# Kernel optimization log

Hardware: AMD Instinct MI355X
Metric: run time of the kernel (lower is better)

Reference implementation:

```python
import jax, jax.numpy as jnp
import numpy as np

N_NODES = 100000
N_EDGES = 1600000
D_FEAT = 32


def setup_inputs() -> dict:
    key = jax.random.key(0)
    k1, k2, k3 = jax.random.split(key, 3)
    features = jax.random.normal(k1, (N_NODES, D_FEAT), dtype=jnp.float32)
    src = jax.random.randint(k2, (N_EDGES,), 0, N_NODES, dtype=jnp.int64)
    dst = jax.random.randint(k3, (N_EDGES,), 0, N_NODES, dtype=jnp.int64)
    return {"features": features, "src": src, "dst": dst}


def reference(features, src, dst):
    # LightConv with norm='both' (default): symmetric degree normalization.
    n = features.shape[0]
    # out-degrees (number of edges leaving each node)
    deg = jnp.zeros((n,), dtype=features.dtype).at[src].add(1.0)
    # norm = deg^-0.5 with inf -> 0 for isolated nodes
    norm = jnp.where(deg > 0, jax.lax.rsqrt(jnp.maximum(deg, 1.0)), 0.0)[:, None]  # [N,1]
    # pre-scale (norm in ['left','both'])
    x = features * norm
    # message = copy_src, reduce = sum over incoming edges
    agg = jax.ops.segment_sum(x[src], dst, num_segments=n)  # [N,D]
    # post-scale (norm in ['right','both']) -- original reads srcdata['norm'],
    # which is the same per-node norm array for a homogeneous graph.
    return agg * norm
```

## Files before the change

kernel.cpp:

```cpp
#include <hip/hip_runtime.h>

#define D_FEAT 32
#define NPB 256
#define NPB_SHIFT 8
#define KMAX 512
#define BPART 512
#define TPART 256
#define SRC_BITS 17
#define SRC_MASK 0x1FFFF
#define CAPI 6144


__global__ __launch_bounds__(TPART) void partition_atomic(const int* __restrict__ src,
                                                          const int* __restrict__ dst,
                                                          int* __restrict__ cntD_g,
                                                          int* __restrict__ cntS_g,
                                                          int* __restrict__ routed_d,
                                                          unsigned char* __restrict__ routed_b,
                                                          int n_edges, int K) {
    __shared__ int hD[KMAX];
    __shared__ int hS[KMAX];
    __shared__ int bD[KMAX];
    __shared__ int bS[KMAX];
    int b = blockIdx.x;
    int tid = threadIdx.x;
    for (int i = tid; i < K; i += TPART) { hD[i] = 0; hS[i] = 0; }
    __syncthreads();
    int chunk = (((n_edges + BPART - 1) / BPART) + 3) & ~3;
    int base = b * chunk;
    int eend = min(base + chunk, n_edges);
    int nvec = (eend > base) ? ((eend - base) >> 2) : 0;
    const int4* d4p = (const int4*)(dst + base);
    const int4* s4p = (const int4*)(src + base);
    for (int i = tid; i < nvec; i += TPART) {
        int4 d4 = d4p[i];
        int4 s4 = s4p[i];
        atomicAdd(&hD[d4.x >> NPB_SHIFT], 1);
        atomicAdd(&hD[d4.y >> NPB_SHIFT], 1);
        atomicAdd(&hD[d4.z >> NPB_SHIFT], 1);
        atomicAdd(&hD[d4.w >> NPB_SHIFT], 1);
        atomicAdd(&hS[s4.x >> NPB_SHIFT], 1);
        atomicAdd(&hS[s4.y >> NPB_SHIFT], 1);
        atomicAdd(&hS[s4.z >> NPB_SHIFT], 1);
        atomicAdd(&hS[s4.w >> NPB_SHIFT], 1);
    }
    for (int e = base + nvec * 4 + tid; e < eend; e += TPART) {
        atomicAdd(&hD[dst[e] >> NPB_SHIFT], 1);
        atomicAdd(&hS[src[e] >> NPB_SHIFT], 1);
    }
    __syncthreads();
    for (int i = tid; i < K; i += TPART) {
        int c = hD[i];
        bD[i] = (c > 0) ? atomicAdd(&cntD_g[i], c) : 0;
        int c2 = hS[i];
        bS[i] = (c2 > 0) ? atomicAdd(&cntS_g[i], c2) : 0;
    }
    __syncthreads();
    for (int i = tid; i < nvec; i += TPART) {
        int4 d4 = d4p[i];
        int4 s4 = s4p[i];
        int dv[4] = {d4.x, d4.y, d4.z, d4.w};
        int sv[4] = {s4.x, s4.y, s4.z, s4.w};
        #pragma unroll
        for (int u = 0; u < 4; u++) {
            int d = dv[u], s = sv[u];
            int kd = d >> NPB_SHIFT;
            int pos = atomicAdd(&bD[kd], 1);
            routed_d[(size_t)kd * CAPI + min(pos, CAPI - 1)] = ((d & (NPB - 1)) << SRC_BITS) | s;
            int ks = s >> NPB_SHIFT;
            int ps = atomicAdd(&bS[ks], 1);
            routed_b[(size_t)ks * CAPI + min(ps, CAPI - 1)] = (unsigned char)(s & (NPB - 1));
        }
    }
    for (int e = base + nvec * 4 + tid; e < eend; e += TPART) {
        int d = dst[e], s = src[e];
        int kd = d >> NPB_SHIFT;
        int pos = atomicAdd(&bD[kd], 1);
        routed_d[(size_t)kd * CAPI + min(pos, CAPI - 1)] = ((d & (NPB - 1)) << SRC_BITS) | s;
        int ks = s >> NPB_SHIFT;
        int ps = atomicAdd(&bS[ks], 1);
        routed_b[(size_t)ks * CAPI + min(ps, CAPI - 1)] = (unsigned char)(s & (NPB - 1));
    }
}

__global__ __launch_bounds__(1024) void mid_kernel(const unsigned char* __restrict__ routed_b,
                                                   const int* __restrict__ routed_d,
                                                   const int* __restrict__ cntS_g,
                                                   const int* __restrict__ cntD_g,
                                                   const float4* __restrict__ feat4,
                                                   float* __restrict__ norm,
                                                   float4* __restrict__ feat_s4,
                                                   int* __restrict__ sorted_src,
                                                   int* __restrict__ row_beg,
                                                   int* __restrict__ row_end,
                                                   int n_nodes, int K) {
    __shared__ int binsS[NPB];
    __shared__ float nrm[NPB];
    __shared__ int bins[NPB];
    __shared__ int sc[NPB];
    __shared__ int cur[NPB];
    int k = blockIdx.x;
    int tid = threadIdx.x;
    int kbase = k << NPB_SHIFT;

    if (tid < NPB) binsS[tid] = 0;
    if (tid < NPB) bins[tid] = 0;
    __syncthreads();
    int begS = k * CAPI;
    int cntS = min(cntS_g[k], CAPI);
    for (int j = tid; j < cntS; j += 1024)
        atomicAdd(&binsS[routed_b[begS + j]], 1);
    int begD = k * CAPI;
    int totD = min(cntD_g[k], CAPI);
    for (int i = tid; i < totD; i += 1024)
        atomicAdd(&bins[routed_d[begD + i] >> SRC_BITS], 1);
    __syncthreads();
    if (tid < NPB) {
        int d = binsS[tid];
        float nv = d > 0 ? rsqrtf((float)d) : 0.0f;
        nrm[tid] = nv;
        int node = kbase + tid;
        if (node < n_nodes) norm[node] = nv;
    }
    if (tid < NPB) sc[tid] = bins[tid];
    __syncthreads();
    for (int st = 1; st < NPB; st <<= 1) {
        int v = (tid < NPB && tid >= st) ? sc[tid - st] : 0;
        __syncthreads();
        if (tid < NPB) sc[tid] += v;
        __syncthreads();
    }
    if (tid < NPB) {
        int ex = sc[tid] - bins[tid];
        cur[tid] = ex;
        int node = kbase + tid;
        if (node < n_nodes) {
            row_beg[node] = begD + ex;
            row_end[node] = begD + sc[tid];
        }
    }
    __syncthreads();
    int base4 = kbase * (D_FEAT / 4);
    for (int i = tid; i < NPB * (D_FEAT / 4); i += 1024) {
        int node = kbase + (i >> 3);
        if (node < n_nodes) {
            float4 v = feat4[base4 + i];
            float nv = nrm[i >> 3];
            v.x *= nv; v.y *= nv; v.z *= nv; v.w *= nv;
            feat_s4[base4 + i] = v;
        }
    }
    for (int i = tid; i < totD; i += 1024) {
        int p = routed_d[begD + i];
        int pos = atomicAdd(&cur[p >> SRC_BITS], 1);
        sorted_src[begD + pos] = p & SRC_MASK;
    }
}

__global__ __launch_bounds__(256) void csr_gather(const float* __restrict__ feat_s,
                                                  const int* __restrict__ sorted_src,
                                                  const int* __restrict__ row_beg,
                                                  const int* __restrict__ row_end,
                                                  const float* __restrict__ norm,
                                                  float* __restrict__ out, int n_nodes) {
    int t = blockIdx.x * blockDim.x + threadIdx.x;
    int node = t >> 5;
    int lane = t & 31;
    if (node >= n_nodes) return;
    int beg = row_beg[node];
    int end = row_end[node];
    float acc = 0.0f;
    for (int base = beg; base < end; base += 32) {
        int idx = min(base + lane, end - 1);
        int sv = sorted_src[idx];
        int m = min(32, end - base);
        int u = 0;
        for (; u + 3 < m; u += 4) {
            int s0 = __shfl(sv, u,     32);
            int s1 = __shfl(sv, u + 1, 32);
            int s2 = __shfl(sv, u + 2, 32);
            int s3 = __shfl(sv, u + 3, 32);
            float a0 = feat_s[s0 * D_FEAT + lane];
            float a1 = feat_s[s1 * D_FEAT + lane];
            float a2 = feat_s[s2 * D_FEAT + lane];
            float a3 = feat_s[s3 * D_FEAT + lane];
            acc += (a0 + a1) + (a2 + a3);
        }
        for (; u < m; u++) {
            int s0 = __shfl(sv, u, 32);
            acc += feat_s[s0 * D_FEAT + lane];
        }
    }
    out[(size_t)node * D_FEAT + lane] = acc * norm[node];
}


__global__ void deg_kernel(const int* __restrict__ src, int* __restrict__ deg, int n_edges) {
    int e = blockIdx.x * blockDim.x + threadIdx.x;
    if (e < n_edges) atomicAdd(&deg[src[e]], 1);
}

__global__ void norm_kernel(const int* __restrict__ deg, float* __restrict__ norm, int n_nodes) {
    int i = blockIdx.x * blockDim.x + threadIdx.x;
    if (i < n_nodes) {
        int d = deg[i];
        norm[i] = d > 0 ? rsqrtf((float)d) : 0.0f;
    }
}

__global__ void scatter_kernel(const float* __restrict__ feat,
                               const int* __restrict__ src,
                               const int* __restrict__ dst,
                               const float* __restrict__ norm,
                               float* __restrict__ out, int n_edges) {
    int t = blockIdx.x * blockDim.x + threadIdx.x;
    int e = t >> 5;
    int d = t & 31;
    if (e < n_edges) {
        int s  = src[e];
        int dd = dst[e];
        float v = feat[s * D_FEAT + d] * norm[s];
        atomicAdd(&out[dd * D_FEAT + d], v);
    }
}

__global__ void post_scale_kernel(float4* __restrict__ out4,
                                  const float* __restrict__ norm, int n4) {
    int t = blockIdx.x * blockDim.x + threadIdx.x;
    if (t < n4) {
        float nv = norm[t >> 3];
        float4 v = out4[t];
        v.x *= nv; v.y *= nv; v.z *= nv; v.w *= nv;
        out4[t] = v;
    }
}


extern "C" void kernel_launch(void* const* d_in, const int* in_sizes, int n_in,
                              void* d_out, int out_size, void* d_ws, size_t ws_size,
                              hipStream_t stream) {
    const float* feat = (const float*)d_in[0];
    const int*   src  = (const int*)d_in[1];
    const int*   dst  = (const int*)d_in[2];
    float* out = (float*)d_out;

    const int n_nodes = in_sizes[0] / D_FEAT;
    const int n_edges = in_sizes[1];
    const int B = 256;

    const int K = (n_nodes + NPB - 1) >> NPB_SHIFT;

    auto align256 = [](size_t x) { return (x + 255) & ~(size_t)255; };
    size_t off = 0;
    size_t cnt_off    = off; off = align256(off + (size_t)2 * K * sizeof(int));
    size_t norm_off   = off; off = align256(off + (size_t)n_nodes * sizeof(float));
    size_t routd_off  = off; off = align256(off + (size_t)K * CAPI * sizeof(int));
    size_t routb_off  = off; off = align256(off + (size_t)K * CAPI * sizeof(unsigned char));
    size_t feats_off  = off; off = align256(off + (size_t)n_nodes * D_FEAT * sizeof(float));
    size_t sortd_off  = off; off = align256(off + (size_t)K * CAPI * sizeof(int));
    size_t rbeg_off   = off; off = align256(off + (size_t)n_nodes * sizeof(int));
    size_t rend_off   = off; off = align256(off + (size_t)n_nodes * sizeof(int));
    size_t needed = off;

    bool ok = (ws_size >= needed) && (K <= KMAX) && (n_nodes <= (1 << SRC_BITS));

    if (ok) {
        int*   cntD_g          = (int*)((char*)d_ws + cnt_off);
        int*   cntS_g          = cntD_g + K;
        float* norm            = (float*)((char*)d_ws + norm_off);
        int*   routed_d        = (int*)((char*)d_ws + routd_off);
        unsigned char* routed_b = (unsigned char*)((char*)d_ws + routb_off);
        float* feat_s          = (float*)((char*)d_ws + feats_off);
        int*   sorted_src      = (int*)((char*)d_ws + sortd_off);
        int*   row_beg         = (int*)((char*)d_ws + rbeg_off);
        int*   row_end         = (int*)((char*)d_ws + rend_off);

        hipMemsetAsync(cntD_g, 0, (size_t)2 * K * sizeof(int), stream);
        partition_atomic<<<BPART, TPART, 0, stream>>>(src, dst, cntD_g, cntS_g,
                                                      routed_d, routed_b, n_edges, K);
        mid_kernel<<<K, 1024, 0, stream>>>(routed_b, routed_d, cntS_g, cntD_g,
                                           (const float4*)feat, norm, (float4*)feat_s,
                                           sorted_src, row_beg, row_end, n_nodes, K);
        long long total = (long long)n_nodes * 32;
        int grid = (int)((total + B - 1) / B);
        csr_gather<<<grid, B, 0, stream>>>(feat_s, sorted_src, row_beg, row_end,
                                           norm, out, n_nodes);
    } else {
        int*   deg  = (int*)d_ws;
        float* norm = (float*)((char*)d_ws + (((size_t)n_nodes * sizeof(int) + 255) & ~(size_t)255));

        hipMemsetAsync(deg, 0, (size_t)n_nodes * sizeof(int), stream);
        hipMemsetAsync(d_out, 0, (size_t)out_size * sizeof(float), stream);

        deg_kernel<<<(n_edges + B - 1) / B, B, 0, stream>>>(src, deg, n_edges);
        norm_kernel<<<(n_nodes + B - 1) / B, B, 0, stream>>>(deg, norm, n_nodes);

        long long total = (long long)n_edges * 32;
        int grid = (int)((total + B - 1) / B);
        scatter_kernel<<<grid, B, 0, stream>>>(feat, src, dst, norm, out, n_edges);

        int n4 = out_size / 4;
        post_scale_kernel<<<(n4 + B - 1) / B, B, 0, stream>>>((float4*)out, norm, n4);
    }
}
```

Measured before the change: 161.2 us.

## Fuse partition, sort and gather into one cooperative persistent kernel

Replaces the memset plus three kernel launches with a single cooperative kernel that uses grid-wide syncs between the partition, per-bucket norm/sort, and CSR gather phases. The goal is to remove launch gaps and the tail effects of each separate kernel. It also changes the work split: the mid-stage tasks are divided into separate source-norm and destination-sort tasks run by 256-thread blocks, and the gather loop runs over nodes persistently. The costs are grid.sync overhead, occupancy limited to whatever fits co-resident, and partition chunks sized by grid count rather than a fixed 512. The old path is kept as a fallback if the cooperative launch fails.

```diff
diff --git a/kernel.cpp b/kernel.cpp
--- a/kernel.cpp
+++ b/kernel.cpp
@@ -1,15 +1,213 @@
 #include <hip/hip_runtime.h>
+#include <hip/hip_cooperative_groups.h>
+
+namespace cg = cooperative_groups;
 
 #define D_FEAT 32
 #define NPB 256
 #define NPB_SHIFT 8
 #define KMAX 512
-#define BPART 512
-#define TPART 256
 #define SRC_BITS 17
 #define SRC_MASK 0x1FFFF
 #define CAPI 6144
-
+#define MAXBLK 1024
+
+__global__ __launch_bounds__(256, 4) void fused_all(const int* __restrict__ src,
+                                                    const int* __restrict__ dst,
+                                                    const float4* __restrict__ feat4,
+                                                    int* __restrict__ cntD_g,
+                                                    int* __restrict__ cntS_g,
+                                                    int* __restrict__ routed_d,
+                                                    unsigned char* __restrict__ routed_b,
+                                                    float* __restrict__ norm,
+                                                    float4* __restrict__ feat_s4,
+                                                    int* __restrict__ sorted_src,
+                                                    int* __restrict__ row_beg,
+                                                    int* __restrict__ row_end,
+                                                    float* __restrict__ out,
+                                                    int n_nodes, int n_edges, int K) {
+    cg::grid_group grid = cg::this_grid();
+    __shared__ int smem[4 * KMAX];
+    int tid = threadIdx.x;
+    int nb = gridDim.x;
+
+    for (int i = blockIdx.x * 256 + tid; i < 2 * K; i += nb * 256) cntD_g[i] = 0;
+    grid.sync();
+
+    {
+        int* hD = smem;
+        int* hS = smem + KMAX;
+        int* bD = smem + 2 * KMAX;
+        int* bS = smem + 3 * KMAX;
+        for (int i = tid; i < K; i += 256) { hD[i] = 0; hS[i] = 0; }
+        __syncthreads();
+        int chunk = (((n_edges + nb - 1) / nb) + 3) & ~3;
+        int base = blockIdx.x * chunk;
+        int eend = min(base + chunk, n_edges);
+        int nvec = (eend > base) ? ((eend - base) >> 2) : 0;
+        const int4* d4p = (const int4*)(dst + base);
+        const int4* s4p = (const int4*)(src + base);
+        for (int i = tid; i < nvec; i += 256) {
+            int4 d4 = d4p[i];
+            int4 s4 = s4p[i];
+            atomicAdd(&hD[d4.x >> NPB_SHIFT], 1);
+            atomicAdd(&hD[d4.y >> NPB_SHIFT], 1);
+            atomicAdd(&hD[d4.z >> NPB_SHIFT], 1);
+            atomicAdd(&hD[d4.w >> NPB_SHIFT], 1);
+            atomicAdd(&hS[s4.x >> NPB_SHIFT], 1);
+            atomicAdd(&hS[s4.y >> NPB_SHIFT], 1);
+            atomicAdd(&hS[s4.z >> NPB_SHIFT], 1);
+            atomicAdd(&hS[s4.w >> NPB_SHIFT], 1);
+        }
+        for (int e = base + nvec * 4 + tid; e < eend; e += 256) {
+            atomicAdd(&hD[dst[e] >> NPB_SHIFT], 1);
+            atomicAdd(&hS[src[e] >> NPB_SHIFT], 1);
+        }
+        __syncthreads();
+        for (int i = tid; i < K; i += 256) {
+            int c = hD[i];
+            bD[i] = (c > 0) ? atomicAdd(&cntD_g[i], c) : 0;
+            int c2 = hS[i];
+            bS[i] = (c2 > 0) ? atomicAdd(&cntS_g[i], c2) : 0;
+        }
+        __syncthreads();
+        for (int i = tid; i < nvec; i += 256) {
+            int4 d4 = d4p[i];
+            int4 s4 = s4p[i];
+            int dv[4] = {d4.x, d4.y, d4.z, d4.w};
+            int sv[4] = {s4.x, s4.y, s4.z, s4.w};
+            #pragma unroll
+            for (int u = 0; u < 4; u++) {
+                int d = dv[u], s = sv[u];
+                int kd = d >> NPB_SHIFT;
+                int pos = atomicAdd(&bD[kd], 1);
+                routed_d[(size_t)kd * CAPI + min(pos, CAPI - 1)] = ((d & (NPB - 1)) << SRC_BITS) | s;
+                int ks = s >> NPB_SHIFT;
+                int ps = atomicAdd(&bS[ks], 1);
+                routed_b[(size_t)ks * CAPI + min(ps, CAPI - 1)] = (unsigned char)(s & (NPB - 1));
+            }
+        }
+        for (int e = base + nvec * 4 + tid; e < eend; e += 256) {
+            int d = dst[e], s = src[e];
+            int kd = d >> NPB_SHIFT;
+            int pos = atomicAdd(&bD[kd], 1);
+            routed_d[(size_t)kd * CAPI + min(pos, CAPI - 1)] = ((d & (NPB - 1)) << SRC_BITS) | s;
+            int ks = s >> NPB_SHIFT;
+            int ps = atomicAdd(&bS[ks], 1);
+            routed_b[(size_t)ks * CAPI + min(ps, CAPI - 1)] = (unsigned char)(s & (NPB - 1));
+        }
+    }
+    grid.sync();
+
+    for (int task = blockIdx.x; task < 2 * K; task += nb) {
+        __syncthreads();
+        if (task < K) {
+            int k = task;
+            int* bins = smem;
+            float* nrm = (float*)(smem + NPB);
+            bins[tid] = 0;
+            __syncthreads();
+            int beg = k * CAPI;
+            int cnt = min(cntS_g[k], CAPI);
+            for (int j = tid; j < cnt; j += 256)
+                atomicAdd(&bins[routed_b[beg + j]], 1);
+            __syncthreads();
+            int kbase = k << NPB_SHIFT;
+            {
+                int d = bins[tid];
+                float nv = d > 0 ? rsqrtf((float)d) : 0.0f;
+                nrm[tid] = nv;
+                int node = kbase + tid;
+                if (node < n_nodes) norm[node] = nv;
+            }
+            __syncthreads();
+            int base4 = kbase * (D_FEAT / 4);
+            for (int i = tid; i < NPB * (D_FEAT / 4); i += 256) {
+                int node = kbase + (i >> 3);
+                if (node < n_nodes) {
+                    float4 v = feat4[base4 + i];
+                    float nv = nrm[i >> 3];
+                    v.x *= nv; v.y *= nv; v.z *= nv; v.w *= nv;
+                    feat_s4[base4 + i] = v;
+                }
+            }
+        } else {
+            int k = task - K;
+            int* bins = smem;
+            int* sc   = smem + NPB;
+            int* cur  = smem + 2 * NPB;
+            bins[tid] = 0;
+            __syncthreads();
+            int beg = k * CAPI;
+            int tot = min(cntD_g[k], CAPI);
+            for (int i = tid; i < tot; i += 256)
+                atomicAdd(&bins[routed_d[beg + i] >> SRC_BITS], 1);
+            __syncthreads();
+            sc[tid] = bins[tid];
+            __syncthreads();
+            for (int st = 1; st < NPB; st <<= 1) {
+                int v = (tid >= st) ? sc[tid - st] : 0;
+                __syncthreads();
+                sc[tid] += v;
+                __syncthreads();
+            }
+            {
+                int ex = sc[tid] - bins[tid];
+                cur[tid] = ex;
+                int node = (k << NPB_SHIFT) + tid;
+                if (node < n_nodes) {
+                    row_beg[node] = beg + ex;
+                    row_end[node] = beg + sc[tid];
+                }
+            }
+            __syncthreads();
+            for (int i = tid; i < tot; i += 256) {
+                int p = routed_d[beg + i];
+                int pos = atomicAdd(&cur[p >> SRC_BITS], 1);
+                sorted_src[beg + pos] = p & SRC_MASK;
+            }
+        }
+    }
+    grid.sync();
+
+    {
+        const float* feat_s = (const float*)feat_s4;
+        int ngroups = nb * 8;
+        int gidx = blockIdx.x * 8 + (tid >> 5);
+        int lane = tid & 31;
+        for (int node = gidx; node < n_nodes; node += ngroups) {
+            int beg = row_beg[node];
+            int end = row_end[node];
+            float acc = 0.0f;
+            for (int base = beg; base < end; base += 32) {
+                int idx = min(base + lane, end - 1);
+                int sv = sorted_src[idx];
+                int m = min(32, end - base);
+                int u = 0;
+                for (; u + 3 < m; u += 4) {
+                    int s0 = __shfl(sv, u,     32);
+                    int s1 = __shfl(sv, u + 1, 32);
+                    int s2 = __shfl(sv, u + 2, 32);
+                    int s3 = __shfl(sv, u + 3, 32);
+                    float a0 = feat_s[s0 * D_FEAT + lane];
+                    float a1 = feat_s[s1 * D_FEAT + lane];
+                    float a2 = feat_s[s2 * D_FEAT + lane];
+                    float a3 = feat_s[s3 * D_FEAT + lane];
+                    acc += (a0 + a1) + (a2 + a3);
+                }
+                for (; u < m; u++) {
+                    int s0 = __shfl(sv, u, 32);
+                    acc += feat_s[s0 * D_FEAT + lane];
+                }
+            }
+            out[(size_t)node * D_FEAT + lane] = acc * norm[node];
+        }
+    }
+}
+
+
+#define BPART 512
+#define TPART 256
 
 __global__ __launch_bounds__(TPART) void partition_atomic(const int* __restrict__ src,
                                                           const int* __restrict__ dst,
@@ -102,9 +300,7 @@
     int k = blockIdx.x;
     int tid = threadIdx.x;
     int kbase = k << NPB_SHIFT;
-
-    if (tid < NPB) binsS[tid] = 0;
-    if (tid < NPB) bins[tid] = 0;
+    if (tid < NPB) { binsS[tid] = 0; bins[tid] = 0; }
     __syncthreads();
     int begS = k * CAPI;
     int cntS = min(cntS_g[k], CAPI);
@@ -275,16 +471,39 @@
         int*   row_beg         = (int*)((char*)d_ws + rbeg_off);
         int*   row_end         = (int*)((char*)d_ws + rend_off);
 
-        hipMemsetAsync(cntD_g, 0, (size_t)2 * K * sizeof(int), stream);
-        partition_atomic<<<BPART, TPART, 0, stream>>>(src, dst, cntD_g, cntS_g,
-                                                      routed_d, routed_b, n_edges, K);
-        mid_kernel<<<K, 1024, 0, stream>>>(routed_b, routed_d, cntS_g, cntD_g,
-                                           (const float4*)feat, norm, (float4*)feat_s,
-                                           sorted_src, row_beg, row_end, n_nodes, K);
-        long long total = (long long)n_nodes * 32;
-        int grid = (int)((total + B - 1) / B);
-        csr_gather<<<grid, B, 0, stream>>>(feat_s, sorted_src, row_beg, row_end,
-                                           norm, out, n_nodes);
+        int blocksPerCU = 0;
+        hipError_t oe = hipOccupancyMaxActiveBlocksPerMultiprocessor(&blocksPerCU,
+                                                                     fused_all, 256, 0);
+        int grid = MAXBLK;
+        if (oe == hipSuccess && blocksPerCU >= 1)
+            grid = min(MAXBLK, blocksPerCU * 256);
+
+        const float4* feat4c = (const float4*)feat;
+        float4* feat_s4 = (float4*)feat_s;
+        int nn = n_nodes, ne = n_edges, kk = K;
+        void* args[] = {
+            (void*)&src, (void*)&dst, (void*)&feat4c,
+            (void*)&cntD_g, (void*)&cntS_g,
+            (void*)&routed_d, (void*)&routed_b,
+            (void*)&norm, (void*)&feat_s4,
+            (void*)&sorted_src, (void*)&row_beg, (void*)&row_end,
+            (void*)&out, (void*)&nn, (void*)&ne, (void*)&kk
+        };
+        hipError_t err = hipLaunchCooperativeKernel((const void*)fused_all,
+                                                    dim3(grid), dim3(256),
+                                                    args, 0, stream);
+        if (err != hipSuccess) {
+            hipMemsetAsync(cntD_g, 0, (size_t)2 * K * sizeof(int), stream);
+            partition_atomic<<<BPART, TPART, 0, stream>>>(src, dst, cntD_g, cntS_g,
+                                                          routed_d, routed_b, n_edges, K);
+            mid_kernel<<<K, 1024, 0, stream>>>(routed_b, routed_d, cntS_g, cntD_g,
+                                               (const float4*)feat, norm, (float4*)feat_s,
+                                               sorted_src, row_beg, row_end, n_nodes, K);
+            long long total = (long long)n_nodes * 32;
+            int grid2 = (int)((total + B - 1) / B);
+            csr_gather<<<grid2, B, 0, stream>>>(feat_s, sorted_src, row_beg, row_end,
+                                                norm, out, n_nodes);
+        }
     } else {
         int*   deg  = (int*)d_ws;
         float* norm = (float*)((char*)d_ws + (((size_t)n_nodes * sizeof(int) + 255) & ~(size_t)255));
```

After: 531.6 us. 230% more time.
